# Kernel tuning notes

Hardware: AMD Instinct MI355X
Metric: run time of the kernel (lower is better)

The kernel has to match this reference:

```python
import jax, jax.numpy as jnp
import numpy as np

B, T, D, H = 4, 2048, 1024, 16

def setup_inputs() -> dict:
    key = jax.random.key(0)
    ks = jax.random.split(key, 5)
    s = 1.0 / np.sqrt(D)
    return {
        "x":  jax.random.normal(ks[0], (B, T, D), dtype=jnp.float32),
        "Wq": jax.random.uniform(ks[1], (D, D), jnp.float32, -s, s),
        "Wk": jax.random.uniform(ks[2], (D, D), jnp.float32, -s, s),
        "Wv": jax.random.uniform(ks[3], (D, D), jnp.float32, -s, s),
        "Wo": jax.random.uniform(ks[4], (D, D), jnp.float32, -s, s),
    }

def reference(x, Wq, Wk, Wv, Wo):
    Bv, Tv, Dv = x.shape
    h = H
    k = Dv // h
    # Linear (no bias): y = x @ W.T, then split heads -> [B, h, T, k]
    Q = (x @ Wq.T).reshape(Bv, Tv, h, k).transpose(0, 2, 1, 3)
    K = (x @ Wk.T).reshape(Bv, Tv, h, k).transpose(0, 2, 1, 3)
    V = (x @ Wv.T).reshape(Bv, Tv, h, k).transpose(0, 2, 1, 3)
    scores = jnp.einsum('bhqk,bhsk->bhqs', Q, K) / jnp.sqrt(jnp.asarray(k, x.dtype))
    causal = jnp.tril(jnp.ones((Tv, Tv), dtype=bool))
    scores = jnp.where(causal[None, None], scores, jnp.asarray(-jnp.inf, x.dtype))
    A = jax.nn.softmax(scores, axis=-1)
    Y = jnp.einsum('bhqs,bhsk->bhqk', A, V).transpose(0, 2, 1, 3).reshape(Bv, Tv, Dv)
    return Y @ Wo.T
```

## Files before the change

### kernel.cpp

```cpp
#include <hip/hip_runtime.h>

typedef __attribute__((ext_vector_type(8))) short short8;
typedef __attribute__((ext_vector_type(4))) float f32x4;
typedef __attribute__((ext_vector_type(2))) unsigned int u32x2;

constexpr int B_ = 4, T_ = 2048, D_ = 1024, H_ = 16;
constexpr int M_ = B_ * T_;
constexpr float SCL2 = 0.1803368801111f;

#if __has_builtin(__builtin_amdgcn_exp2f)
#define EXP2F __builtin_amdgcn_exp2f
#else
#define EXP2F exp2f
#endif

#define DEV __device__ __forceinline__

DEV unsigned short f2bf(float f) {
  unsigned int u = __builtin_bit_cast(unsigned int, f);
  u += 0x7FFFu + ((u >> 16) & 1u);
  return (unsigned short)(u >> 16);
}

DEV void gload16(const unsigned short* g, unsigned short* l) {
  __builtin_amdgcn_global_load_lds(
      (const __attribute__((address_space(1))) unsigned int*)g,
      (__attribute__((address_space(3))) unsigned int*)l, 16, 0, 0);
}

__global__ __launch_bounds__(256) void cvt_all(const float* __restrict__ x,
                                               const float* __restrict__ w0, const float* __restrict__ w1,
                                               const float* __restrict__ w2, const float* __restrict__ w3,
                                               unsigned short* __restrict__ xb,
                                               unsigned short* __restrict__ o0, unsigned short* __restrict__ o1,
                                               unsigned short* __restrict__ o2, unsigned short* __restrict__ o3) {
  int b = blockIdx.x;
  const float* in;
  unsigned short* out;
  int blk;
  if (b < 8192) { in = x; out = xb; blk = b; }
  else {
    int s = (b - 8192) >> 10;
    blk = (b - 8192) & 1023;
    in  = s == 0 ? w0 : s == 1 ? w1 : s == 2 ? w2 : w3;
    out = s == 0 ? o0 : s == 1 ? o1 : s == 2 ? o2 : o3;
  }
  int i = (blk * 256 + threadIdx.x) * 4;
  float4 f = *(const float4*)(in + i);
  ushort4 o;
  o.x = f2bf(f.x); o.y = f2bf(f.y); o.z = f2bf(f.z); o.w = f2bf(f.w);
  *(ushort4*)(out + i) = o;
}

template <int OUTMODE>
__global__ __launch_bounds__(256, 2) void gemm_bt(const unsigned short* __restrict__ A,
                                                  const unsigned short* __restrict__ B,
                                                  void* __restrict__ C,
                                                  int M, int N, int K) {
  constexpr int BM = 128, BN = 128, BK = 64;
  __shared__ __align__(16) unsigned short a_sh[2 * BM * BK];
  __shared__ __align__(16) unsigned short b_sh[2 * BN * BK];

  const int tid = threadIdx.x;
  const int lane = tid & 63;
  const int w = tid >> 6;
  const int l15 = lane & 15, lg = lane >> 4;
  const int wr = w >> 1, wc = w & 1;

  const int nwg = gridDim.x;
  const int swz = (blockIdx.x & 7) * (nwg >> 3) + (blockIdx.x >> 3);

  const int NT = N / BN;
  const int tm = swz / NT, tn = swz % NT;
  const unsigned short* Ab = A + (size_t)tm * BM * K;
  const unsigned short* Bb = B + (size_t)tn * BN * K;

  f32x4 acc[4][4];
#pragma unroll
  for (int m = 0; m < 4; ++m)
#pragma unroll
    for (int n = 0; n < 4; ++n) acc[m][n] = (f32x4){0.f, 0.f, 0.f, 0.f};

  auto stage = [&](int buf, int kt) {
    int k0 = kt * BK;
#pragma unroll
    for (int rnd = 0; rnd < 4; ++rnd) {
      int c = rnd * 256 + tid;
      int row = c >> 3, s = c & 7;
      int koff = k0 + 8 * (s ^ (row & 7));
      unsigned short* ldst_a = a_sh + buf * BM * BK + (rnd * 256 + w * 64) * 8;
      unsigned short* ldst_b = b_sh + buf * BN * BK + (rnd * 256 + w * 64) * 8;
      gload16(Ab + (size_t)row * K + koff, ldst_a);
      gload16(Bb + (size_t)row * K + koff, ldst_b);
    }
  };

  stage(0, 0);
  int cur = 0;
  const int NK = K / BK;
  for (int kt = 0; kt < NK; ++kt) {
    __syncthreads();
    if (kt + 1 < NK) stage(cur ^ 1, kt + 1);
    const unsigned short* ab = a_sh + cur * BM * BK;
    const unsigned short* bb = b_sh + cur * BN * BK;
#pragma unroll
    for (int kk = 0; kk < 2; ++kk) {
      short8 af[4], bf8[4];
#pragma unroll
      for (int m = 0; m < 4; ++m) {
        int row = wr * 64 + m * 16 + l15;
        int slot = (kk * 4 + lg) ^ (row & 7);
        af[m] = *(const short8*)(ab + row * 64 + slot * 8);
      }
#pragma unroll
      for (int n = 0; n < 4; ++n) {
        int row = wc * 64 + n * 16 + l15;
        int slot = (kk * 4 + lg) ^ (row & 7);
        bf8[n] = *(const short8*)(bb + row * 64 + slot * 8);
      }
#pragma unroll
      for (int m = 0; m < 4; ++m)
#pragma unroll
        for (int n = 0; n < 4; ++n)
          acc[m][n] = __builtin_amdgcn_mfma_f32_16x16x32_bf16(af[m], bf8[n], acc[m][n], 0, 0, 0);
    }
    cur ^= 1;
  }

  const int row0 = tm * BM + wr * 64 + lg * 4;
  const int col0 = tn * BN + wc * 64 + l15;
#pragma unroll
  for (int m = 0; m < 4; ++m)
#pragma unroll
    for (int n = 0; n < 4; ++n) {
      if (OUTMODE == 3) {
        const int region = tn >> 3;
        const int nc = col0 - (region << 10) + n * 16;
        const int mm = row0 + m * 16;
        if (region == 2) {
          size_t base = (size_t)2 * 8388608 +
                        ((size_t)((mm >> 11) * 16 + (nc >> 6))) * 131072 +
                        (size_t)(nc & 63) * 2048 + (mm & 2047);
          ushort4 pk;
          pk.x = f2bf(acc[m][n][0]); pk.y = f2bf(acc[m][n][1]);
          pk.z = f2bf(acc[m][n][2]); pk.w = f2bf(acc[m][n][3]);
          *(ushort4*)((unsigned short*)C + base) = pk;
        } else {
          unsigned short* dst = (unsigned short*)C + (size_t)region * 8388608;
#pragma unroll
          for (int r = 0; r < 4; ++r)
            dst[(size_t)(mm + r) * 1024 + nc] = f2bf(acc[m][n][r]);
        }
      } else {
#pragma unroll
        for (int r = 0; r < 4; ++r) {
          size_t idx = (size_t)(row0 + m * 16 + r) * N + (col0 + n * 16);
          if (OUTMODE == 1)
            ((float*)C)[idx] = acc[m][n][r];
          else
            ((unsigned short*)C)[idx] = f2bf(acc[m][n][r]);
        }
      }
    }
}

__global__ __launch_bounds__(256, 3) void attn(const unsigned short* __restrict__ Q,
                                               const unsigned short* __restrict__ K,
                                               const unsigned short* __restrict__ Vt,
                                               unsigned short* __restrict__ Y) {
  __shared__ __align__(16) unsigned short k_sh[2][64 * 64];
  __shared__ __align__(16) unsigned short v_sh[2][64 * 64];
  __shared__ __align__(16) unsigned short p_sh[4][32][72];

  const int tid = threadIdx.x;
  const int lane = tid & 63;
  const int w = tid >> 6;
  const int l15 = lane & 15, lg = lane >> 4;

  const int bid = blockIdx.x;
  const int qt_blk = 15 - (bid >> 6);
  const int bh = (bid & 7) * 8 + ((bid >> 3) & 7);
  const int h = bh & 15;
  const int b = bh >> 4;
  const int q0 = qt_blk * 128;
  const int qq0 = q0 + 32 * w;

  const unsigned short* Qp = Q + ((size_t)(b * T_ + q0)) * D_ + h * 64;
  const unsigned short* Kp = K + ((size_t)(b * T_)) * D_ + h * 64;
  const unsigned short* Vtp = Vt + (size_t)bh * 131072;

  auto stK = [&](int buf, int kv0) {
#pragma unroll
    for (int j = 0; j < 2; ++j) {
      int c = j * 256 + tid;
      int row = c >> 3;
      gload16(Kp + (size_t)(kv0 + row) * D_ + 8 * ((c & 7) ^ (row & 7)),
              &k_sh[buf][(j * 256 + w * 64) * 8]);
    }
  };
  auto stV = [&](int buf, int kv0) {
#pragma unroll
    for (int j = 0; j < 2; ++j) {
      int c = j * 256 + tid;
      int d = c >> 3;
      gload16(Vtp + (size_t)d * 2048 + kv0 + 8 * ((c & 7) ^ (d & 7)),
              &v_sh[buf][(j * 256 + w * 64) * 8]);
    }
  };

  short8 qf[2][2];
#pragma unroll
  for (int qt = 0; qt < 2; ++qt)
#pragma unroll
    for (int kk = 0; kk < 2; ++kk)
      qf[qt][kk] = *(const short8*)(Qp + (size_t)(32 * w + 16 * qt + l15) * D_ + 32 * kk + 8 * lg);

  stK(0, 0);
  stV(0, 0);
  __syncthreads();

  unsigned short* p_w = &p_sh[w][0][0];

  const float NEGINF = -__builtin_inff();
  float ml[2] = {NEGINF, NEGINF};
  float ll[2] = {0.f, 0.f};
  f32x4 o[2][4];
#pragma unroll
  for (int qt = 0; qt < 2; ++qt)
#pragma unroll
    for (int t = 0; t < 4; ++t) o[qt][t] = (f32x4){0.f, 0.f, 0.f, 0.f};

  const int NI = 2 * qt_blk + 2;
  int cur = 0;
  for (int i = 0; i < NI; ++i) {
    const int kv0 = i * 64;
    if (i + 1 < NI) { stK(cur ^ 1, kv0 + 64); stV(cur ^ 1, kv0 + 64); }

    const bool active = (kv0 <= qq0 + 31);
    if (active) {
      f32x4 sacc[2][4];
#pragma unroll
      for (int qt = 0; qt < 2; ++qt)
#pragma unroll
        for (int t = 0; t < 4; ++t) sacc[qt][t] = (f32x4){0.f, 0.f, 0.f, 0.f};
      const char* kb = (const char*)k_sh[cur];
      __builtin_amdgcn_s_setprio(1);
#pragma unroll
      for (int t = 0; t < 4; ++t) {
        int sr = 16 * t + l15;
        int sw = (sr & 7) << 4;
        short8 kf0 = *(const short8*)(kb + sr * 128 + ((16 * lg) ^ sw));
        short8 kf1 = *(const short8*)(kb + sr * 128 + ((64 + 16 * lg) ^ sw));
#pragma unroll
        for (int qt = 0; qt < 2; ++qt) {
          sacc[qt][t] = __builtin_amdgcn_mfma_f32_16x16x32_bf16(kf0, qf[qt][0], sacc[qt][t], 0, 0, 0);
          sacc[qt][t] = __builtin_amdgcn_mfma_f32_16x16x32_bf16(kf1, qf[qt][1], sacc[qt][t], 0, 0, 0);
        }
      }
      __builtin_amdgcn_s_setprio(0);

      float corr[2];
      bool defer[2];
#pragma unroll
      for (int qt = 0; qt < 2; ++qt) {
        const bool nomask = (kv0 + 63) <= (qq0 + 16 * qt);
        float sv[16];
        if (nomask) {
#pragma unroll
          for (int t = 0; t < 4; ++t)
#pragma unroll
            for (int r = 0; r < 4; ++r) sv[4 * t + r] = sacc[qt][t][r];
        } else {
          const int qg = qq0 + 16 * qt + l15;
#pragma unroll
          for (int t = 0; t < 4; ++t)
#pragma unroll
            for (int r = 0; r < 4; ++r) {
              int sg = kv0 + 16 * t + 4 * lg + r;
              sv[4 * t + r] = (sg <= qg) ? sacc[qt][t][r] : NEGINF;
            }
        }
        float a8[8], a4[4], a2[2];
#pragma unroll
        for (int k = 0; k < 8; ++k) a8[k] = fmaxf(sv[k], sv[k + 8]);
#pragma unroll
        for (int k = 0; k < 4; ++k) a4[k] = fmaxf(a8[k], a8[k + 4]);
        a2[0] = fmaxf(a4[0], a4[2]); a2[1] = fmaxf(a4[1], a4[3]);
        float mx = fmaxf(a2[0], a2[1]);
        mx = fmaxf(mx, __shfl_xor(mx, 16));
        mx = fmaxf(mx, __shfl_xor(mx, 32));
        defer[qt] = (__all(mx <= ml[qt] + 8.0f) != 0);
        float mnew = defer[qt] ? ml[qt] : fmaxf(ml[qt], mx);
        corr[qt] = defer[qt] ? 1.0f : EXP2F((ml[qt] - mnew) * SCL2);
        float nms2 = mnew * SCL2;
        float pv[16];
#pragma unroll
        for (int k = 0; k < 16; ++k) pv[k] = EXP2F(fmaf(sv[k], SCL2, -nms2));
        float s8[8], s4[4], s2[2];
#pragma unroll
        for (int k = 0; k < 8; ++k) s8[k] = pv[k] + pv[k + 8];
#pragma unroll
        for (int k = 0; k < 4; ++k) s4[k] = s8[k] + s8[k + 4];
        s2[0] = s4[0] + s4[2]; s2[1] = s4[1] + s4[3];
        float ps = s2[0] + s2[1];
        ps += __shfl_xor(ps, 16);
        ps += __shfl_xor(ps, 32);
        ll[qt] = ll[qt] * corr[qt] + ps;
        ml[qt] = mnew;
#pragma unroll
        for (int t = 0; t < 4; ++t) {
          unsigned lo, hi;
          asm("v_cvt_pk_bf16_f32 %0, %1, %2" : "=v"(lo) : "v"(pv[4 * t]), "v"(pv[4 * t + 1]));
          asm("v_cvt_pk_bf16_f32 %0, %1, %2" : "=v"(hi) : "v"(pv[4 * t + 2]), "v"(pv[4 * t + 3]));
          u32x2 pk = {lo, hi};
          *(u32x2*)(void*)(p_w + (16 * qt + l15) * 72 + 16 * t + 4 * lg) = pk;
        }
      }
      asm volatile("" ::: "memory");

#pragma unroll
      for (int qt = 0; qt < 2; ++qt)
        if (!defer[qt]) {
#pragma unroll
          for (int r = 0; r < 4; ++r) {
            float cr = __shfl(corr[qt], 4 * lg + r);
#pragma unroll
            for (int t = 0; t < 4; ++t) o[qt][t][r] *= cr;
          }
        }

      short8 pa[2][2];
#pragma unroll
      for (int qt = 0; qt < 2; ++qt)
#pragma unroll
        for (int kk = 0; kk < 2; ++kk)
          pa[qt][kk] = *(const short8*)(p_w + (16 * qt + l15) * 72 + kk * 32 + 8 * lg);

      const char* vbT = (const char*)v_sh[cur];
      __builtin_amdgcn_s_setprio(1);
#pragma unroll
      for (int t = 0; t < 4; ++t) {
        int dr = 16 * t + l15;
        int sw = (dr & 7) << 4;
        short8 vf0 = *(const short8*)(vbT + dr * 128 + ((16 * lg) ^ sw));
        short8 vf1 = *(const short8*)(vbT + dr * 128 + ((64 + 16 * lg) ^ sw));
#pragma unroll
        for (int qt = 0; qt < 2; ++qt) {
          o[qt][t] = __builtin_amdgcn_mfma_f32_16x16x32_bf16(pa[qt][0], vf0, o[qt][t], 0, 0, 0);
          o[qt][t] = __builtin_amdgcn_mfma_f32_16x16x32_bf16(pa[qt][1], vf1, o[qt][t], 0, 0, 0);
        }
      }
      __builtin_amdgcn_s_setprio(0);
    }
    __syncthreads();
    cur ^= 1;
  }

#pragma unroll
  for (int qt = 0; qt < 2; ++qt) {
    float linv = 1.0f / ll[qt];
#pragma unroll
    for (int r = 0; r < 4; ++r) {
      float li = __shfl(linv, 4 * lg + r);
      int qg = qq0 + 16 * qt + 4 * lg + r;
      unsigned short* Yp = Y + ((size_t)(b * T_ + qg)) * D_ + h * 64;
#pragma unroll
      for (int t = 0; t < 4; ++t)
        Yp[16 * t + l15] = f2bf(o[qt][t][r] * li);
    }
  }
}

extern "C" void kernel_launch(void* const* d_in, const int* in_sizes, int n_in,
                              void* d_out, int out_size, void* d_ws, size_t ws_size,
                              hipStream_t stream) {
  const float* x  = (const float*)d_in[0];
  const float* Wq = (const float*)d_in[1];
  const float* Wk = (const float*)d_in[2];
  const float* Wv = (const float*)d_in[3];
  const float* Wo = (const float*)d_in[4];
  float* out = (float*)d_out;

  const size_t NX = (size_t)M_ * D_;
  const size_t NW = (size_t)D_ * D_;
  const size_t need = (4 * NX + 4 * NW) * sizeof(unsigned short);
  if (ws_size < need) return;

  unsigned short* ws  = (unsigned short*)d_ws;
  unsigned short* xb  = ws;
  unsigned short* wqb = xb + NX;
  unsigned short* wkb = wqb + NW;
  unsigned short* wvb = wkb + NW;
  unsigned short* wob = wvb + NW;
  unsigned short* Qb  = wob + NW;
  unsigned short* Yb  = xb;

  cvt_all<<<12288, 256, 0, stream>>>(x, Wq, Wk, Wv, Wo, xb, wqb, wkb, wvb, wob);

  gemm_bt<3><<<(M_ / 128) * (3072 / 128), 256, 0, stream>>>(xb, wqb, Qb, M_, 3072, D_);

  attn<<<B_ * H_ * (T_ / 128), 256, 0, stream>>>(Qb, Qb + NX, Qb + 2 * NX, Yb);

  gemm_bt<1><<<(M_ / 128) * (D_ / 128), 256, 0, stream>>>(Yb, wob, out, M_, D_, D_);
}
```

Before: 164.8 us.

## Replace full syncthreads with partial vmcnt waits to overlap next-tile loads

In both the GEMM and the attention loops, the end-of-iteration __syncthreads (which drains all outstanding global-to-LDS loads) is replaced. Each iteration now starts with a raw barrier, issues the next stage's async loads, and waits only until the previous stage's loads have landed (vmcnt counting the new ones as outstanding), then barriers again. This lets the prefetch for the next tile stay in flight while the current tile is computed, instead of being drained every iteration. It relies on the vmcnt constants matching the exact number of load instructions per stage. It also adds sched_barriers that limit compiler reordering.

```diff
diff --git a/kernel.cpp b/kernel.cpp
--- a/kernel.cpp
+++ b/kernel.cpp
@@ -99,8 +99,19 @@
   int cur = 0;
   const int NK = K / BK;
   for (int kt = 0; kt < NK; ++kt) {
-    __syncthreads();
-    if (kt + 1 < NK) stage(cur ^ 1, kt + 1);
+    __builtin_amdgcn_s_barrier();
+    __builtin_amdgcn_sched_barrier(0);
+    if (kt + 1 < NK) {
+      stage(cur ^ 1, kt + 1);
+      __builtin_amdgcn_sched_barrier(0);
+      asm volatile("s_waitcnt vmcnt(8)" ::: "memory");
+    } else {
+      asm volatile("s_waitcnt vmcnt(0)" ::: "memory");
+    }
+    __builtin_amdgcn_sched_barrier(0);
+    __builtin_amdgcn_s_barrier();
+    __builtin_amdgcn_sched_barrier(0);
+
     const unsigned short* ab = a_sh + cur * BM * BK;
     const unsigned short* bb = b_sh + cur * BN * BK;
 #pragma unroll
@@ -217,7 +228,6 @@
 
   stK(0, 0);
   stV(0, 0);
-  __syncthreads();
 
   unsigned short* p_w = &p_sh[w][0][0];
 
@@ -234,7 +244,19 @@
   int cur = 0;
   for (int i = 0; i < NI; ++i) {
     const int kv0 = i * 64;
-    if (i + 1 < NI) { stK(cur ^ 1, kv0 + 64); stV(cur ^ 1, kv0 + 64); }
+    __builtin_amdgcn_s_barrier();
+    __builtin_amdgcn_sched_barrier(0);
+    if (i + 1 < NI) {
+      stK(cur ^ 1, kv0 + 64);
+      stV(cur ^ 1, kv0 + 64);
+      __builtin_amdgcn_sched_barrier(0);
+      asm volatile("s_waitcnt vmcnt(4)" ::: "memory");
+    } else {
+      asm volatile("s_waitcnt vmcnt(0)" ::: "memory");
+    }
+    __builtin_amdgcn_sched_barrier(0);
+    __builtin_amdgcn_s_barrier();
+    __builtin_amdgcn_sched_barrier(0);
 
     const bool active = (kv0 <= qq0 + 31);
     if (active) {
@@ -352,7 +374,6 @@
       }
       __builtin_amdgcn_s_setprio(0);
     }
-    __syncthreads();
     cur ^= 1;
   }
 
```

After: 164.4 us. About the same (-0.3%).
